# Performance work log

Measured on AMD Instinct MI355X. Metric: run time of the kernel, lower is better.

Reference implementation:

```python
import jax, jax.numpy as jnp
import numpy as np


def _grid_sample_3d(vol, grid):
    """Trilinear grid_sample, align_corners=True, zeros padding.
    vol: (b, c, D, H, W); grid: (b, D, H, W, 3) with last dim = (x, y, z)
    where x indexes W, y indexes H, z indexes D (torch convention)."""
    b, c, D, H, W = vol.shape
    dt = vol.dtype
    ix = (grid[..., 0] + 1.0) * 0.5 * (W - 1)
    iy = (grid[..., 1] + 1.0) * 0.5 * (H - 1)
    iz = (grid[..., 2] + 1.0) * 0.5 * (D - 1)
    ix0 = jnp.floor(ix); iy0 = jnp.floor(iy); iz0 = jnp.floor(iz)
    fx = ix - ix0; fy = iy - iy0; fz = iz - iz0

    def gather(v, zi, yi, xi):  # v: (c,D,H,W); indices: (D,H,W)
        return v[:, zi, yi, xi]  # -> (c,D,H,W)

    out = jnp.zeros((b, c, D, H, W), dt)
    for dz in (0, 1):
        z = iz0 + dz
        wz = fz if dz else (1.0 - fz)
        vz = (z >= 0) & (z <= D - 1)
        zi = jnp.clip(z, 0, D - 1).astype(jnp.int32)
        for dy in (0, 1):
            yc = iy0 + dy
            wy = fy if dy else (1.0 - fy)
            vy = (yc >= 0) & (yc <= H - 1)
            yi = jnp.clip(yc, 0, H - 1).astype(jnp.int32)
            for dx in (0, 1):
                xc = ix0 + dx
                wx = fx if dx else (1.0 - fx)
                vx = (xc >= 0) & (xc <= W - 1)
                xi = jnp.clip(xc, 0, W - 1).astype(jnp.int32)
                wgt = (wz * wy * wx) * (vz & vy & vx).astype(dt)  # (b,D,H,W)
                vals = jax.vmap(gather)(vol, zi, yi, xi)          # (b,c,D,H,W)
                out = out + vals * wgt[:, None]
    return out


def _forward(x, y):
    b, c, h, w, d = x.shape
    dt = x.dtype
    # identity affine_grid coordinates (align_corners=True):
    # grid[...,0] varies along innermost axis d, [...,1] along w, [...,2] along h
    gx = jnp.linspace(-1.0, 1.0, d, dtype=dt)[None, None, None, :]
    gy = jnp.linspace(-1.0, 1.0, w, dtype=dt)[None, None, :, None]
    gz = jnp.linspace(-1.0, 1.0, h, dtype=dt)[None, :, None, None]

    x0 = x[:, 0]  # (b,h,w,d), channel 0 as in the torch code
    y0 = y[:, 0]
    x_sum = jnp.sum(x)  # global sums, matching torch.sum over all elements
    y_sum = jnp.sum(y)

    tx = jnp.sum(x0 * gx) / x_sum - jnp.sum(y0 * gx) / y_sum
    ty = jnp.sum(x0 * gy) / x_sum - jnp.sum(y0 * gy) / y_sum
    tz = jnp.sum(x0 * gz) / x_sum - jnp.sum(y0 * gz) / y_sum

    shp = (b, h, w, d)
    grid = jnp.stack([
        jnp.broadcast_to(gx + tx, shp),
        jnp.broadcast_to(gy + ty, shp),
        jnp.broadcast_to(gz + tz, shp),
    ], axis=-1)  # (b,h,w,d,3)

    transformed = _grid_sample_3d(x, grid)
    return transformed, grid


def setup_inputs() -> dict:
    key = jax.random.key(0)
    k1, k2 = jax.random.split(key)
    shape = (2, 1, 192, 192, 192)
    x = jax.random.uniform(k1, shape, dtype=jnp.float32)
    y = jax.random.uniform(k2, shape, dtype=jnp.float32)
    return {"x": x, "y": y}


def reference(x, y):
    return _forward(x, y)
```

## Files before the change

kernel.cpp:

```cpp
#include <hip/hip_runtime.h>

static constexpr int DIM    = 192;
static constexpr int NVOX   = 2 * DIM * DIM * DIM;
static constexpr int N4     = NVOX / 4;
static constexpr int TSIZE  = NVOX;
static constexpr int RBLOCKS = 2048;

__global__ __launch_bounds__(256) void com_reduce(const float* __restrict__ x,
                                                  const float* __restrict__ y,
                                                  float* __restrict__ ws) {
    const float step = 2.0f / 191.0f;
    float a0 = 0, a1 = 0, a2 = 0, a3 = 0;
    float b0 = 0, b1 = 0, b2 = 0, b3 = 0;

    for (int t = blockIdx.x * blockDim.x + threadIdx.x; t < N4;
         t += gridDim.x * blockDim.x) {
        int idx = t * 4;
        int k = idx % DIM;
        int r = idx / DIM;
        int j = r % DIM;
        int i = (r / DIM) % DIM;

        float4 xv = reinterpret_cast<const float4*>(x)[t];
        float4 yv = reinterpret_cast<const float4*>(y)[t];

        float gj = fmaf((float)j, step, -1.0f);
        float gi = fmaf((float)i, step, -1.0f);
        float g0 = fmaf((float)(k + 0), step, -1.0f);
        float g1 = fmaf((float)(k + 1), step, -1.0f);
        float g2 = fmaf((float)(k + 2), step, -1.0f);
        float g3 = fmaf((float)(k + 3), step, -1.0f);

        float xs  = (xv.x + xv.y) + (xv.z + xv.w);
        float ys  = (yv.x + yv.y) + (yv.z + yv.w);
        float xgx = xv.x * g0 + xv.y * g1 + xv.z * g2 + xv.w * g3;
        float ygx = yv.x * g0 + yv.y * g1 + yv.z * g2 + yv.w * g3;

        a0 += xs;  a1 += xgx;  a2 += xs * gj;  a3 += xs * gi;
        b0 += ys;  b1 += ygx;  b2 += ys * gj;  b3 += ys * gi;
    }

    float v[8] = {a0, a1, a2, a3, b0, b1, b2, b3};
#pragma unroll
    for (int q = 0; q < 8; ++q) {
#pragma unroll
        for (int off = 32; off > 0; off >>= 1)
            v[q] += __shfl_down(v[q], off, 64);
    }

    __shared__ float sm[4][8];
    int lane = threadIdx.x & 63;
    int wave = threadIdx.x >> 6;
    if (lane == 0) {
#pragma unroll
        for (int q = 0; q < 8; ++q) sm[wave][q] = v[q];
    }
    __syncthreads();
    if (threadIdx.x < 8) {
        float s = sm[0][threadIdx.x] + sm[1][threadIdx.x] +
                  sm[2][threadIdx.x] + sm[3][threadIdx.x];
        ws[16 + blockIdx.x * 8 + threadIdx.x] = s;
    }
}

__global__ __launch_bounds__(256) void com_finalize(float* __restrict__ ws) {
    __shared__ double sd[256];
    int t = threadIdx.x;
    int q = t & 7;
    double s = 0;
    for (int p = t >> 3; p < RBLOCKS; p += 32)
        s += (double)ws[16 + p * 8 + q];
    sd[t] = s;
    __syncthreads();
    for (int off = 128; off >= 8; off >>= 1) {
        if (t < off) sd[t] += sd[t + off];
        __syncthreads();
    }
    if (t == 0) {
        double xs = sd[0], xgx = sd[1], xgy = sd[2], xgz = sd[3];
        double ys = sd[4], ygx = sd[5], ygy = sd[6], ygz = sd[7];
        double tx = xgx / xs - ygx / ys;
        double ty = xgy / xs - ygy / ys;
        double tz = xgz / xs - ygz / ys;
        double sx = tx * 95.5, sy = ty * 95.5, sz = tz * 95.5;
        double fsx = floor(sx), fsy = floor(sy), fsz = floor(sz);
        ws[0] = (float)(sx - fsx);
        ws[1] = (float)(sy - fsy);
        ws[2] = (float)(sz - fsz);
        ws[3] = (float)tx;
        ws[4] = (float)ty;
        ws[5] = (float)tz;
        int* ip = reinterpret_cast<int*>(ws + 6);
        ip[0] = (int)fsx; ip[1] = (int)fsy; ip[2] = (int)fsz;
    }
}

__global__ __launch_bounds__(192) void com_apply(const float* __restrict__ x,
                                                 float* __restrict__ out,
                                                 const float* __restrict__ ws) {
    float fx = ws[0], fy = ws[1], fz = ws[2];
    float txf = ws[3], tyf = ws[4], tzf = ws[5];
    const int* ip = reinterpret_cast<const int*>(ws + 6);
    int iox = ip[0], ioy = ip[1], ioz = ip[2];

    int bid = blockIdx.x;
    int jg = bid % 48;
    int i  = (bid / 48) % DIM;
    int b  = bid / (48 * DIM);
    int j0 = jg * 4;
    int tid = threadIdx.x;

    int z0 = i + ioz, z1 = z0 + 1;
    float wz0 = (z0 >= 0 && z0 < DIM) ? 1.0f - fz : 0.0f;
    float wz1 = (z1 >= 0 && z1 < DIM) ? fz : 0.0f;
    int zc0 = min(max(z0, 0), DIM - 1), zc1 = min(max(z1, 0), DIM - 1);

    __shared__ float srow[5][240];

    for (int p = tid; p < 240; p += 192) {
        int m = p / 48, cc = p % 48;
        int col = (cc < 16) ? cc : (cc - 16 + 208);
        srow[m][col] = 0.0f;
    }

    const float* xb = x + (size_t)b * (DIM * DIM * DIM);
#pragma unroll 2
    for (int task = tid; task < 240; task += 192) {
        int m = task / 48;
        int c = (task % 48) * 4;
        int yv = j0 + ioy + m;
        int yc = min(max(yv, 0), DIM - 1);
        const float* p0 = xb + (zc0 * DIM + yc) * DIM + c;
        const float* p1 = xb + (zc1 * DIM + yc) * DIM + c;
        float4 va = *reinterpret_cast<const float4*>(p0);
        float4 vb = *reinterpret_cast<const float4*>(p1);
        float4 s;
        s.x = wz0 * va.x + wz1 * vb.x;
        s.y = wz0 * va.y + wz1 * vb.y;
        s.z = wz0 * va.z + wz1 * vb.z;
        s.w = wz0 * va.w + wz1 * vb.w;
        *reinterpret_cast<float4*>(&srow[m][16 + c]) = s;
    }
    __syncthreads();

    int rr = tid / 48;
    int k4 = tid % 48;
    int k  = k4 * 4;
    int j  = j0 + rr;
    int yv0 = j + ioy, yv1 = yv0 + 1;
    float wy0 = (yv0 >= 0 && yv0 < DIM) ? 1.0f - fy : 0.0f;
    float wy1 = (yv1 >= 0 && yv1 < DIM) ? fy : 0.0f;

    float wx0[4], wx1[4];
#pragma unroll
    for (int m = 0; m < 4; ++m) {
        int c0 = k + m + iox, c1 = c0 + 1;
        wx0[m] = (c0 >= 0 && c0 < DIM) ? 1.0f - fx : 0.0f;
        wx1[m] = (c1 >= 0 && c1 < DIM) ? fx : 0.0f;
    }

    int a  = iox & 3;
    int cb = 16 + k + (iox - a);
    float f0[8], f1[8];
    *reinterpret_cast<float4*>(&f0[0]) = *reinterpret_cast<const float4*>(&srow[rr][cb]);
    *reinterpret_cast<float4*>(&f0[4]) = *reinterpret_cast<const float4*>(&srow[rr][cb + 4]);
    *reinterpret_cast<float4*>(&f1[0]) = *reinterpret_cast<const float4*>(&srow[rr + 1][cb]);
    *reinterpret_cast<float4*>(&f1[4]) = *reinterpret_cast<const float4*>(&srow[rr + 1][cb + 4]);

    float res[4];
#define DOCASE(A)                                                           \
    _Pragma("unroll")                                                       \
    for (int m = 0; m < 4; ++m) {                                           \
        float u0 = wy0 * f0[A + m]     + wy1 * f1[A + m];                   \
        float u1 = wy0 * f0[A + m + 1] + wy1 * f1[A + m + 1];               \
        res[m] = wx0[m] * u0 + wx1[m] * u1;                                 \
    }
    switch (a) {
        case 0: DOCASE(0); break;
        case 1: DOCASE(1); break;
        case 2: DOCASE(2); break;
        default: DOCASE(3); break;
    }
#undef DOCASE

    reinterpret_cast<float4*>(out)[bid * 192 + tid] =
        make_float4(res[0], res[1], res[2], res[3]);

    const float step = 2.0f / 191.0f;
    float gzv = fmaf((float)i, step, -1.0f) + tzf;
    int g4base = TSIZE / 4 + bid * 576;
#pragma unroll
    for (int s = 0; s < 3; ++s) {
        float4 gv;
#pragma unroll
        for (int u = 0; u < 4; ++u) {
            int L = (tid + s * 192) * 4 + u;
            int lv = L / 3;
            int comp = L - lv * 3;
            int kk = lv % DIM;
            int rj = lv / DIM;
            float val;
            if (comp == 0)      val = fmaf((float)kk, step, -1.0f) + txf;
            else if (comp == 1) val = fmaf((float)(j0 + rj), step, -1.0f) + tyf;
            else                val = gzv;
            reinterpret_cast<float*>(&gv)[u] = val;
        }
        reinterpret_cast<float4*>(out)[g4base + tid + s * 192] = gv;
    }
}

extern "C" void kernel_launch(void* const* d_in, const int* in_sizes, int n_in,
                              void* d_out, int out_size, void* d_ws, size_t ws_size,
                              hipStream_t stream) {
    const float* x = (const float*)d_in[0];
    const float* y = (const float*)d_in[1];
    float* out = (float*)d_out;
    float* ws = (float*)d_ws;

    com_reduce<<<RBLOCKS, 256, 0, stream>>>(x, y, ws);
    com_finalize<<<1, 256, 0, stream>>>(ws);
    com_apply<<<NVOX / 768, 192, 0, stream>>>(x, out, ws);
}
```

Before: 92.50 us.

## Fold finalize into apply kernel, widen reduce and apply tiles, use nontemporal I/O

```diff
diff --git a/kernel.cpp b/kernel.cpp
--- a/kernel.cpp
+++ b/kernel.cpp
@@ -1,43 +1,51 @@
 #include <hip/hip_runtime.h>
 
-static constexpr int DIM    = 192;
-static constexpr int NVOX   = 2 * DIM * DIM * DIM;
-static constexpr int N4     = NVOX / 4;
-static constexpr int TSIZE  = NVOX;
-static constexpr int RBLOCKS = 2048;
-
-__global__ __launch_bounds__(256) void com_reduce(const float* __restrict__ x,
-                                                  const float* __restrict__ y,
-                                                  float* __restrict__ ws) {
+typedef float f4 __attribute__((ext_vector_type(4)));
+
+static constexpr int DIM     = 192;
+static constexpr int NVOX    = 2 * DIM * DIM * DIM;
+static constexpr int N8      = NVOX / 8;
+static constexpr int TSIZE   = NVOX;
+static constexpr int RBLOCKS = 256;
+static constexpr int RTHREADS = 1024;
+
+__global__ __launch_bounds__(1024) void com_reduce(const float* __restrict__ x,
+                                                   const float* __restrict__ y,
+                                                   float* __restrict__ ws) {
     const float step = 2.0f / 191.0f;
     float a0 = 0, a1 = 0, a2 = 0, a3 = 0;
     float b0 = 0, b1 = 0, b2 = 0, b3 = 0;
 
-    for (int t = blockIdx.x * blockDim.x + threadIdx.x; t < N4;
-         t += gridDim.x * blockDim.x) {
-        int idx = t * 4;
+    for (int t8 = blockIdx.x * RTHREADS + threadIdx.x; t8 < N8;
+         t8 += RBLOCKS * RTHREADS) {
+        int idx = t8 * 8;
         int k = idx % DIM;
         int r = idx / DIM;
         int j = r % DIM;
         int i = (r / DIM) % DIM;
 
-        float4 xv = reinterpret_cast<const float4*>(x)[t];
-        float4 yv = reinterpret_cast<const float4*>(y)[t];
-
+        const f4* xp = reinterpret_cast<const f4*>(x) + t8 * 2;
+        const f4* yp = reinterpret_cast<const f4*>(y) + t8 * 2;
+        f4 x0 = __builtin_nontemporal_load(xp);
+        f4 x1 = __builtin_nontemporal_load(xp + 1);
+        f4 y0 = __builtin_nontemporal_load(yp);
+        f4 y1 = __builtin_nontemporal_load(yp + 1);
+
+        float g[8];
+#pragma unroll
+        for (int u = 0; u < 8; ++u) g[u] = fmaf((float)(k + u), step, -1.0f);
         float gj = fmaf((float)j, step, -1.0f);
         float gi = fmaf((float)i, step, -1.0f);
-        float g0 = fmaf((float)(k + 0), step, -1.0f);
-        float g1 = fmaf((float)(k + 1), step, -1.0f);
-        float g2 = fmaf((float)(k + 2), step, -1.0f);
-        float g3 = fmaf((float)(k + 3), step, -1.0f);
-
-        float xs  = (xv.x + xv.y) + (xv.z + xv.w);
-        float ys  = (yv.x + yv.y) + (yv.z + yv.w);
-        float xgx = xv.x * g0 + xv.y * g1 + xv.z * g2 + xv.w * g3;
-        float ygx = yv.x * g0 + yv.y * g1 + yv.z * g2 + yv.w * g3;
-
-        a0 += xs;  a1 += xgx;  a2 += xs * gj;  a3 += xs * gi;
-        b0 += ys;  b1 += ygx;  b2 += ys * gj;  b3 += ys * gi;
+
+        float xs = ((x0.x + x0.y) + (x0.z + x0.w)) + ((x1.x + x1.y) + (x1.z + x1.w));
+        float ys = ((y0.x + y0.y) + (y0.z + y0.w)) + ((y1.x + y1.y) + (y1.z + y1.w));
+        float xg = ((x0.x * g[0] + x0.y * g[1]) + (x0.z * g[2] + x0.w * g[3]))
+                 + ((x1.x * g[4] + x1.y * g[5]) + (x1.z * g[6] + x1.w * g[7]));
+        float yg = ((y0.x * g[0] + y0.y * g[1]) + (y0.z * g[2] + y0.w * g[3]))
+                 + ((y1.x * g[4] + y1.y * g[5]) + (y1.z * g[6] + y1.w * g[7]));
+
+        a0 += xs;  a1 += xg;  a2 += xs * gj;  a3 += xs * gi;
+        b0 += ys;  b1 += yg;  b2 += ys * gj;  b3 += ys * gi;
     }
 
     float v[8] = {a0, a1, a2, a3, b0, b1, b2, b3};
@@ -48,7 +56,7 @@
             v[q] += __shfl_down(v[q], off, 64);
     }
 
-    __shared__ float sm[4][8];
+    __shared__ float sm[16][8];
     int lane = threadIdx.x & 63;
     int wave = threadIdx.x >> 6;
     if (lane == 0) {
@@ -57,89 +65,92 @@
     }
     __syncthreads();
     if (threadIdx.x < 8) {
-        float s = sm[0][threadIdx.x] + sm[1][threadIdx.x] +
-                  sm[2][threadIdx.x] + sm[3][threadIdx.x];
-        ws[16 + blockIdx.x * 8 + threadIdx.x] = s;
+        float s = 0;
+#pragma unroll
+        for (int w = 0; w < 16; ++w) s += sm[w][threadIdx.x];
+        ws[blockIdx.x * 8 + threadIdx.x] = s;
     }
 }
 
-__global__ __launch_bounds__(256) void com_finalize(float* __restrict__ ws) {
-    __shared__ double sd[256];
-    int t = threadIdx.x;
-    int q = t & 7;
-    double s = 0;
-    for (int p = t >> 3; p < RBLOCKS; p += 32)
-        s += (double)ws[16 + p * 8 + q];
-    sd[t] = s;
-    __syncthreads();
-    for (int off = 128; off >= 8; off >>= 1) {
-        if (t < off) sd[t] += sd[t + off];
-        __syncthreads();
-    }
-    if (t == 0) {
-        double xs = sd[0], xgx = sd[1], xgy = sd[2], xgz = sd[3];
-        double ys = sd[4], ygx = sd[5], ygy = sd[6], ygz = sd[7];
-        double tx = xgx / xs - ygx / ys;
-        double ty = xgy / xs - ygy / ys;
-        double tz = xgz / xs - ygz / ys;
+__global__ __launch_bounds__(384) void com_apply(const float* __restrict__ x,
+                                                 float* __restrict__ out,
+                                                 const float* __restrict__ wsp) {
+    __shared__ double sd[6][8];
+    __shared__ float  sp[16];
+    __shared__ float  srow[9][240];
+
+    int tid = threadIdx.x;
+
+    for (int p = tid; p < 432; p += 384) {
+        int m = p / 48, cc = p % 48;
+        int col = (cc < 16) ? cc : (cc - 16 + 208);
+        srow[m][col] = 0.0f;
+    }
+
+    {
+        double s = 0;
+        for (int idx = tid; idx < RBLOCKS * 8; idx += 384)
+            s += (double)wsp[idx];
+        s += __shfl_xor(s, 8, 64);
+        s += __shfl_xor(s, 16, 64);
+        s += __shfl_xor(s, 32, 64);
+        int lane = tid & 63, wave = tid >> 6;
+        if (lane < 8) sd[wave][lane] = s;
+    }
+    __syncthreads();
+    if (tid == 0) {
+        double t[8];
+#pragma unroll
+        for (int q = 0; q < 8; ++q) {
+            double s = 0;
+#pragma unroll
+            for (int w = 0; w < 6; ++w) s += sd[w][q];
+            t[q] = s;
+        }
+        double tx = t[1] / t[0] - t[5] / t[4];
+        double ty = t[2] / t[0] - t[6] / t[4];
+        double tz = t[3] / t[0] - t[7] / t[4];
         double sx = tx * 95.5, sy = ty * 95.5, sz = tz * 95.5;
         double fsx = floor(sx), fsy = floor(sy), fsz = floor(sz);
-        ws[0] = (float)(sx - fsx);
-        ws[1] = (float)(sy - fsy);
-        ws[2] = (float)(sz - fsz);
-        ws[3] = (float)tx;
-        ws[4] = (float)ty;
-        ws[5] = (float)tz;
-        int* ip = reinterpret_cast<int*>(ws + 6);
+        sp[0] = (float)(sx - fsx);
+        sp[1] = (float)(sy - fsy);
+        sp[2] = (float)(sz - fsz);
+        sp[3] = (float)tx;
+        sp[4] = (float)ty;
+        sp[5] = (float)tz;
+        int* ip = reinterpret_cast<int*>(sp + 6);
         ip[0] = (int)fsx; ip[1] = (int)fsy; ip[2] = (int)fsz;
     }
-}
-
-__global__ __launch_bounds__(192) void com_apply(const float* __restrict__ x,
-                                                 float* __restrict__ out,
-                                                 const float* __restrict__ ws) {
-    float fx = ws[0], fy = ws[1], fz = ws[2];
-    float txf = ws[3], tyf = ws[4], tzf = ws[5];
-    const int* ip = reinterpret_cast<const int*>(ws + 6);
+    __syncthreads();
+
+    float fx = sp[0], fy = sp[1], fz = sp[2];
+    float txf = sp[3], tyf = sp[4], tzf = sp[5];
+    const int* ip = reinterpret_cast<const int*>(sp + 6);
     int iox = ip[0], ioy = ip[1], ioz = ip[2];
 
     int bid = blockIdx.x;
-    int jg = bid % 48;
-    int i  = (bid / 48) % DIM;
-    int b  = bid / (48 * DIM);
-    int j0 = jg * 4;
-    int tid = threadIdx.x;
+    int jg = bid % 24;
+    int i  = (bid / 24) % DIM;
+    int b  = bid / (24 * DIM);
+    int j0 = jg * 8;
 
     int z0 = i + ioz, z1 = z0 + 1;
     float wz0 = (z0 >= 0 && z0 < DIM) ? 1.0f - fz : 0.0f;
     float wz1 = (z1 >= 0 && z1 < DIM) ? fz : 0.0f;
     int zc0 = min(max(z0, 0), DIM - 1), zc1 = min(max(z1, 0), DIM - 1);
 
-    __shared__ float srow[5][240];
-
-    for (int p = tid; p < 240; p += 192) {
-        int m = p / 48, cc = p % 48;
-        int col = (cc < 16) ? cc : (cc - 16 + 208);
-        srow[m][col] = 0.0f;
-    }
-
     const float* xb = x + (size_t)b * (DIM * DIM * DIM);
-#pragma unroll 2
-    for (int task = tid; task < 240; task += 192) {
+    for (int task = tid; task < 432; task += 384) {
         int m = task / 48;
         int c = (task % 48) * 4;
         int yv = j0 + ioy + m;
         int yc = min(max(yv, 0), DIM - 1);
-        const float* p0 = xb + (zc0 * DIM + yc) * DIM + c;
-        const float* p1 = xb + (zc1 * DIM + yc) * DIM + c;
-        float4 va = *reinterpret_cast<const float4*>(p0);
-        float4 vb = *reinterpret_cast<const float4*>(p1);
-        float4 s;
-        s.x = wz0 * va.x + wz1 * vb.x;
-        s.y = wz0 * va.y + wz1 * vb.y;
-        s.z = wz0 * va.z + wz1 * vb.z;
-        s.w = wz0 * va.w + wz1 * vb.w;
-        *reinterpret_cast<float4*>(&srow[m][16 + c]) = s;
+        const f4* p0 = reinterpret_cast<const f4*>(xb + (zc0 * DIM + yc) * DIM + c);
+        const f4* p1 = reinterpret_cast<const f4*>(xb + (zc1 * DIM + yc) * DIM + c);
+        f4 va = *p0;
+        f4 vb = *p1;
+        f4 s = wz0 * va + wz1 * vb;
+        *reinterpret_cast<f4*>(&srow[m][16 + c]) = s;
     }
     __syncthreads();
 
@@ -162,10 +173,10 @@
     int a  = iox & 3;
     int cb = 16 + k + (iox - a);
     float f0[8], f1[8];
-    *reinterpret_cast<float4*>(&f0[0]) = *reinterpret_cast<const float4*>(&srow[rr][cb]);
-    *reinterpret_cast<float4*>(&f0[4]) = *reinterpret_cast<const float4*>(&srow[rr][cb + 4]);
-    *reinterpret_cast<float4*>(&f1[0]) = *reinterpret_cast<const float4*>(&srow[rr + 1][cb]);
-    *reinterpret_cast<float4*>(&f1[4]) = *reinterpret_cast<const float4*>(&srow[rr + 1][cb + 4]);
+    *reinterpret_cast<f4*>(&f0[0]) = *reinterpret_cast<const f4*>(&srow[rr][cb]);
+    *reinterpret_cast<f4*>(&f0[4]) = *reinterpret_cast<const f4*>(&srow[rr][cb + 4]);
+    *reinterpret_cast<f4*>(&f1[0]) = *reinterpret_cast<const f4*>(&srow[rr + 1][cb]);
+    *reinterpret_cast<f4*>(&f1[4]) = *reinterpret_cast<const f4*>(&srow[rr + 1][cb + 4]);
 
     float res[4];
 #define DOCASE(A)                                                           \
@@ -183,18 +194,18 @@
     }
 #undef DOCASE
 
-    reinterpret_cast<float4*>(out)[bid * 192 + tid] =
-        make_float4(res[0], res[1], res[2], res[3]);
+    f4 tr = {res[0], res[1], res[2], res[3]};
+    __builtin_nontemporal_store(tr, reinterpret_cast<f4*>(out) + bid * 384 + tid);
 
     const float step = 2.0f / 191.0f;
     float gzv = fmaf((float)i, step, -1.0f) + tzf;
-    int g4base = TSIZE / 4 + bid * 576;
+    int g4base = TSIZE / 4 + bid * 1152;
 #pragma unroll
     for (int s = 0; s < 3; ++s) {
-        float4 gv;
+        f4 gv;
 #pragma unroll
         for (int u = 0; u < 4; ++u) {
-            int L = (tid + s * 192) * 4 + u;
+            int L = (tid + s * 384) * 4 + u;
             int lv = L / 3;
             int comp = L - lv * 3;
             int kk = lv % DIM;
@@ -203,9 +214,9 @@
             if (comp == 0)      val = fmaf((float)kk, step, -1.0f) + txf;
             else if (comp == 1) val = fmaf((float)(j0 + rj), step, -1.0f) + tyf;
             else                val = gzv;
-            reinterpret_cast<float*>(&gv)[u] = val;
+            gv[u] = val;
         }
-        reinterpret_cast<float4*>(out)[g4base + tid + s * 192] = gv;
+        __builtin_nontemporal_store(gv, reinterpret_cast<f4*>(out) + g4base + tid + s * 384);
     }
 }
 
@@ -217,7 +228,6 @@
     float* out = (float*)d_out;
     float* ws = (float*)d_ws;
 
-    com_reduce<<<RBLOCKS, 256, 0, stream>>>(x, y, ws);
-    com_finalize<<<1, 256, 0, stream>>>(ws);
-    com_apply<<<NVOX / 768, 192, 0, stream>>>(x, out, ws);
+    com_reduce<<<RBLOCKS, RTHREADS, 0, stream>>>(x, y, ws);
+    com_apply<<<NVOX / 1536, 384, 0, stream>>>(x, out, ws);
 }
```

New measurement: 93.65 us. Within noise of the previous version (+1.2%).
